# Kernel tuning notes

Measured on AMD Instinct MI355X. Metric: run time of the kernel, lower is better.

Reference implementation:

```python
import jax, jax.numpy as jnp
import numpy as np


def soft_threshold24(w):
    """2:4 soft-threshold along the last dim: in each contiguous group of 4,
    zero the two smallest magnitudes and shrink the two largest by the
    second-smallest magnitude (sign(w) * relu(|w| - t))."""
    M, N = w.shape
    g = w.reshape(M, N // 4, 4)
    a = jnp.abs(g)
    thr = jnp.sort(a, axis=-1)[..., 1:2]  # 2nd-smallest magnitude per group
    s = jnp.sign(g) * jnp.maximum(a - thr, 0.0)
    return s.reshape(M, N)


def mm_fp16(a, b):
    """fake_fp8_mm: cast operands to fp16, accumulate in fp32."""
    return jnp.matmul(a.astype(jnp.float16), b.astype(jnp.float16),
                      preferred_element_type=jnp.float32)


def setup_inputs() -> dict:
    key = jax.random.key(0)
    k0, k1, k2, k3 = jax.random.split(key, 4)
    B, S, D, R = 4, 2048, 2048, 512
    return {
        "x": jax.random.normal(k0, (B, S, D), jnp.float32),
        "weight_in": jax.random.normal(k1, (D, R), jnp.float32) * 0.02,
        "weight_out": jax.random.normal(k2, (D, R), jnp.float32) * 0.02,
        "bias": jax.random.normal(k3, (D,), jnp.float32) * 0.01,
        "sparse_scale_in": jnp.array(1.0, jnp.float32),
        "sparse_scale_out": jnp.array(1.0, jnp.float32),
    }


def reference(x, weight_in, weight_out, bias, sparse_scale_in, sparse_scale_out):
    B, S, D = x.shape
    # stage 1: x @ sparse24(weight_in) * scale_in  -> [B,S,R]
    win_s = soft_threshold24(weight_in) * sparse_scale_in          # [D, R]
    h = mm_fp16(x.reshape(-1, D), win_s)                            # [B*S, R] fp32
    # stage 2: h @ sparse24(weight_out.T) * scale_out + bias -> [B,S,D]
    wout_s = soft_threshold24(weight_out.T) * sparse_scale_out      # [R, D]
    out = mm_fp16(h, wout_s) + bias                                 # [B*S, D]
    return out.reshape(B, S, D)
```

## Files before the change

### kernel.cpp

```cpp
#include <hip/hip_runtime.h>

typedef _Float16 f16;
typedef _Float16 f16x8 __attribute__((ext_vector_type(8)));
typedef float f32x4 __attribute__((ext_vector_type(4)));

#define BK 32

__device__ __forceinline__ void g2l16(const void* g, void* l) {
    __builtin_amdgcn_global_load_lds(
        (const __attribute__((address_space(1))) void*)g,
        (__attribute__((address_space(3))) void*)l, 16, 0, 0);
}

template <int N> __device__ __forceinline__ void wait_vmcnt();
template <> __device__ __forceinline__ void wait_vmcnt<0>() { asm volatile("s_waitcnt vmcnt(0)" ::: "memory"); }
template <> __device__ __forceinline__ void wait_vmcnt<4>() { asm volatile("s_waitcnt vmcnt(4)" ::: "memory"); }

__device__ __forceinline__ float soft1(float a, float thr, float w, float s) {
    return copysignf(fmaxf(a - thr, 0.0f), w) * s;
}

__device__ __forceinline__ float thr4(float a0, float a1, float a2, float a3) {
    float lo01 = fminf(a0, a1), hi01 = fmaxf(a0, a1);
    float lo23 = fminf(a2, a3), hi23 = fmaxf(a2, a3);
    return fminf(fmaxf(lo01, lo23), fminf(hi01, hi23));
}

__global__ __launch_bounds__(256) void prep_kernel(
    const float* __restrict__ Wi, f16* __restrict__ winT, const float* __restrict__ sci,
    const float* __restrict__ Wo, f16* __restrict__ woutT, const float* __restrict__ sco,
    int D, int R, int nSpInB)
{
    int b = blockIdx.x;
    int tid = threadIdx.x;
    if (b < nSpInB) {
        int t = b * 256 + tid;
        int RG = R >> 2;
        if (t >= RG * D) return;
        int rg = t / D, d = t - rg * D;
        float s = *sci;
        float4 w = *reinterpret_cast<const float4*>(Wi + (size_t)d * R + rg * 4);
        float a0 = fabsf(w.x), a1 = fabsf(w.y), a2 = fabsf(w.z), a3 = fabsf(w.w);
        float thr = thr4(a0, a1, a2, a3);
        size_t base = (size_t)(rg * 4) * D + d;
        winT[base]                 = (f16)soft1(a0, thr, w.x, s);
        winT[base + D]             = (f16)soft1(a1, thr, w.y, s);
        winT[base + 2 * (size_t)D] = (f16)soft1(a2, thr, w.z, s);
        winT[base + 3 * (size_t)D] = (f16)soft1(a3, thr, w.w, s);
    } else {
        int t = (b - nSpInB) * 256 + tid;
        if (t >= (D >> 2) * R) return;
        int dg = t / R, r = t - dg * R;
        float s = *sco;
        size_t i0 = (size_t)(dg * 4) * R + r;
        float w0 = Wo[i0], w1 = Wo[i0 + R], w2 = Wo[i0 + 2 * (size_t)R], w3 = Wo[i0 + 3 * (size_t)R];
        float a0 = fabsf(w0), a1 = fabsf(w1), a2 = fabsf(w2), a3 = fabsf(w3);
        float thr = thr4(a0, a1, a2, a3);
        woutT[i0]                 = (f16)soft1(a0, thr, w0, s);
        woutT[i0 + R]             = (f16)soft1(a1, thr, w1, s);
        woutT[i0 + 2 * (size_t)R] = (f16)soft1(a2, thr, w2, s);
        woutT[i0 + 3 * (size_t)R] = (f16)soft1(a3, thr, w3, s);
    }
}

template <int TBM, int TBN, typename AT, typename OT, bool BIAS>
__global__ __launch_bounds__(256) void gemm_bt(
    const AT* __restrict__ A, const f16* __restrict__ Bt, OT* __restrict__ C,
    const float* __restrict__ bias, int M, int N, int K)
{
    constexpr bool AF32 = sizeof(AT) == 4;
    constexpr int MI = TBM / 32;
    constexpr int NF = TBN / 32;
    constexpr int HM = TBM / 2;
    constexpr int HN = TBN / 2;
    constexpr int LA = TBM * BK * (int)sizeof(AT) / 4096;
    constexpr int LB = TBN * BK * 2 / 4096;
    constexpr int L  = LA + LB;
    static_assert(L == 4, "wait_vmcnt<L> instantiations assume L==4");
    __shared__ AT  As[2][TBM * BK];
    __shared__ f16 Bs[2][TBN * BK];

    const int tid  = threadIdx.x;
    const int lane = tid & 63;
    const int w    = tid >> 6;
    const int wm   = w & 1;
    const int wn   = w >> 1;
    const int l16  = lane & 15;
    const int quad = lane >> 4;

    const int nbx = N / TBN;
    const int nb  = gridDim.x;
    int d = blockIdx.x;
    int wgid = ((nb & 7) == 0) ? ((d & 7) * (nb >> 3) + (d >> 3)) : d;
    int by = wgid / nbx;
    int bx = wgid - by * nbx;
    const int bm = by * TBM;
    const int bn = bx * TBN;

    const int srow = lane >> 2;
    const int scol = (lane & 3) * 8;
    const f16* gB = Bt + (size_t)(bn + w * (TBN / 4) + srow) * K + scol;

    const int srowA = AF32 ? (lane >> 3) : srow;
    const int scolA = AF32 ? (((lane & 7) ^ (lane >> 3)) * 4) : scol;
    const AT* gA = A + (size_t)(bm + w * (TBM / 4) + srowA) * K + scolA;

    f32x4 acc[MI][NF] = {};

    auto STAGE = [&](int buf, int t) {
        const int k0 = t * BK;
        AT*  lA = &As[buf][(w * (TBM / 4)) * BK];
        f16* lB = &Bs[buf][(w * (TBN / 4)) * BK];
        if constexpr (AF32) {
#pragma unroll
            for (int i = 0; i < (TBM / 4) / 8; ++i)
                g2l16(gA + k0 + i * 8 * (size_t)K, lA + i * 8 * BK);
        } else {
#pragma unroll
            for (int i = 0; i < (TBM / 4) / 16; ++i)
                g2l16(gA + k0 + i * 16 * (size_t)K, lA + i * 16 * BK);
        }
#pragma unroll
        for (int i = 0; i < (TBN / 4) / 16; ++i)
            g2l16(gB + k0 + i * 16 * (size_t)K, lB + i * 16 * BK);
    };

    auto LOADFRAG = [&](int buf, f16x8* af, f16x8* bf) {
        if constexpr (AF32) {
#pragma unroll
            for (int m = 0; m < MI; ++m) {
                int lr = wm * HM + m * 16 + l16;
                const char* row = reinterpret_cast<const char*>(&As[buf][lr * BK]);
                int swz = (lr & 7) << 4;
                f32x4 lo = *reinterpret_cast<const f32x4*>(row + (((quad * 32)      ) ^ swz));
                f32x4 hi = *reinterpret_cast<const f32x4*>(row + (((quad * 32) + 16 ) ^ swz));
                f16x8 a;
#pragma unroll
                for (int j = 0; j < 4; ++j) { a[j] = (f16)lo[j]; a[j + 4] = (f16)hi[j]; }
                af[m] = a;
            }
        } else {
#pragma unroll
            for (int m = 0; m < MI; ++m)
                af[m] = *reinterpret_cast<const f16x8*>(
                    &As[buf][(wm * HM + m * 16 + l16) * BK + quad * 8]);
        }
#pragma unroll
        for (int n = 0; n < NF; ++n)
            bf[n] = *reinterpret_cast<const f16x8*>(
                &Bs[buf][(wn * HN + n * 16 + l16) * BK + quad * 8]);
    };

    auto MFMA_ALL = [&](f16x8* af, f16x8* bf) {
#pragma unroll
        for (int m = 0; m < MI; ++m)
#pragma unroll
            for (int n = 0; n < NF; ++n)
                acc[m][n] = __builtin_amdgcn_mfma_f32_16x16x32_f16(af[m], bf[n], acc[m][n], 0, 0, 0);
    };

    const int nk = K / BK;
    STAGE(0, 0);
    STAGE(1, 1);
    for (int t = 0; t < nk - 2; ++t) {
        wait_vmcnt<4>();
        __builtin_amdgcn_s_barrier();
        __builtin_amdgcn_sched_barrier(0);
        f16x8 af[MI], bf[NF];
        LOADFRAG(t & 1, af, bf);
        asm volatile("s_waitcnt lgkmcnt(0)" ::: "memory");
        __builtin_amdgcn_sched_barrier(0);
        __builtin_amdgcn_s_barrier();
        STAGE(t & 1, t + 2);
        MFMA_ALL(af, bf);
    }
    {
        wait_vmcnt<4>();
        __builtin_amdgcn_s_barrier();
        __builtin_amdgcn_sched_barrier(0);
        f16x8 af[MI], bf[NF];
        LOADFRAG(nk & 1, af, bf);
        MFMA_ALL(af, bf);
    }
    {
        wait_vmcnt<0>();
        __builtin_amdgcn_s_barrier();
        __builtin_amdgcn_sched_barrier(0);
        f16x8 af[MI], bf[NF];
        LOADFRAG((nk - 1) & 1, af, bf);
        MFMA_ALL(af, bf);
    }

#pragma unroll
    for (int m = 0; m < MI; ++m) {
        int row_base = bm + wm * HM + m * 16 + quad * 4;
#pragma unroll
        for (int n = 0; n < NF; ++n) {
            int col = bn + wn * HN + n * 16 + l16;
            float b = BIAS ? bias[col] : 0.0f;
#pragma unroll
            for (int r = 0; r < 4; ++r) {
                float v = acc[m][n][r];
                size_t idx = (size_t)(row_base + r) * N + col;
                if constexpr (BIAS) C[idx] = (OT)(v + b);
                else                C[idx] = (OT)v;
            }
        }
    }
}

extern "C" void kernel_launch(void* const* d_in, const int* in_sizes, int n_in,
                              void* d_out, int out_size, void* d_ws, size_t ws_size,
                              hipStream_t stream)
{
    const float* x      = (const float*)d_in[0];
    const float* w_in   = (const float*)d_in[1];
    const float* w_out  = (const float*)d_in[2];
    const float* bias   = (const float*)d_in[3];
    const float* sc_in  = (const float*)d_in[4];
    const float* sc_out = (const float*)d_in[5];

    const int D = in_sizes[3];
    const int R = in_sizes[1] / D;
    const int M = in_sizes[0] / D;

    f16* winT  = (f16*)d_ws;
    f16* woutT = winT + (size_t)R * D;
    f16* h     = woutT + (size_t)D * R;
    float* out = (float*)d_out;

    const int nSpInB  = ((R / 4) * D + 255) / 256;
    const int nSpOutB = ((D / 4) * R + 255) / 256;
    prep_kernel<<<nSpInB + nSpOutB, 256, 0, stream>>>(
        w_in, winT, sc_in, w_out, woutT, sc_out, D, R, nSpInB);

    gemm_bt<64, 128, float, f16, false><<<(R / 128) * (M / 64), 256, 0, stream>>>(
        x, winT, h, nullptr, M, R, D);
    gemm_bt<128, 128, f16, float, true><<<(D / 128) * (M / 128), 256, 0, stream>>>(
        h, woutT, out, bias, M, D, R);
}
```

Before: 197.6 us.

## Stage fp32 A via registers, converting to fp16 before LDS write

For the fp32-input GEMM (stage 1), A tiles are no longer copied straight from global memory into LDS as fp32. They are now loaded into registers, converted to fp16 once, and written to LDS as fp16. This halves the LDS footprint and LDS read traffic for A, and removes the repeated per-fragment fp32-to-fp16 conversion. In exchange it adds register staging, a manually unrolled two-buffer loop with extra barriers and lgkmcnt waits, and loses the asynchronous direct-to-LDS path for A.

```diff
diff --git a/kernel.cpp b/kernel.cpp
--- a/kernel.cpp
+++ b/kernel.cpp
@@ -73,11 +73,7 @@
     constexpr int NF = TBN / 32;
     constexpr int HM = TBM / 2;
     constexpr int HN = TBN / 2;
-    constexpr int LA = TBM * BK * (int)sizeof(AT) / 4096;
-    constexpr int LB = TBN * BK * 2 / 4096;
-    constexpr int L  = LA + LB;
-    static_assert(L == 4, "wait_vmcnt<L> instantiations assume L==4");
-    __shared__ AT  As[2][TBM * BK];
+    __shared__ f16 As[2][TBM * BK];
     __shared__ f16 Bs[2][TBN * BK];
 
     const int tid  = threadIdx.x;
@@ -100,51 +96,23 @@
     const int srow = lane >> 2;
     const int scol = (lane & 3) * 8;
     const f16* gB = Bt + (size_t)(bn + w * (TBN / 4) + srow) * K + scol;
-
-    const int srowA = AF32 ? (lane >> 3) : srow;
-    const int scolA = AF32 ? (((lane & 7) ^ (lane >> 3)) * 4) : scol;
-    const AT* gA = A + (size_t)(bm + w * (TBM / 4) + srowA) * K + scolA;
+    const AT*  gA = A  + (size_t)(bm + w * (TBM / 4) + srow) * K + scol;
+    const int  aoff = (w * (TBM / 4) + srow) * BK + scol;
 
     f32x4 acc[MI][NF] = {};
 
-    auto STAGE = [&](int buf, int t) {
-        const int k0 = t * BK;
-        AT*  lA = &As[buf][(w * (TBM / 4)) * BK];
+    auto STAGE_B = [&](int buf, int t) {
         f16* lB = &Bs[buf][(w * (TBN / 4)) * BK];
-        if constexpr (AF32) {
-#pragma unroll
-            for (int i = 0; i < (TBM / 4) / 8; ++i)
-                g2l16(gA + k0 + i * 8 * (size_t)K, lA + i * 8 * BK);
-        } else {
-#pragma unroll
-            for (int i = 0; i < (TBM / 4) / 16; ++i)
-                g2l16(gA + k0 + i * 16 * (size_t)K, lA + i * 16 * BK);
-        }
 #pragma unroll
         for (int i = 0; i < (TBN / 4) / 16; ++i)
-            g2l16(gB + k0 + i * 16 * (size_t)K, lB + i * 16 * BK);
+            g2l16(gB + (size_t)t * BK + i * 16 * (size_t)K, lB + i * 16 * BK);
     };
 
     auto LOADFRAG = [&](int buf, f16x8* af, f16x8* bf) {
-        if constexpr (AF32) {
-#pragma unroll
-            for (int m = 0; m < MI; ++m) {
-                int lr = wm * HM + m * 16 + l16;
-                const char* row = reinterpret_cast<const char*>(&As[buf][lr * BK]);
-                int swz = (lr & 7) << 4;
-                f32x4 lo = *reinterpret_cast<const f32x4*>(row + (((quad * 32)      ) ^ swz));
-                f32x4 hi = *reinterpret_cast<const f32x4*>(row + (((quad * 32) + 16 ) ^ swz));
-                f16x8 a;
-#pragma unroll
-                for (int j = 0; j < 4; ++j) { a[j] = (f16)lo[j]; a[j + 4] = (f16)hi[j]; }
-                af[m] = a;
-            }
-        } else {
-#pragma unroll
-            for (int m = 0; m < MI; ++m)
-                af[m] = *reinterpret_cast<const f16x8*>(
-                    &As[buf][(wm * HM + m * 16 + l16) * BK + quad * 8]);
-        }
+#pragma unroll
+        for (int m = 0; m < MI; ++m)
+            af[m] = *reinterpret_cast<const f16x8*>(
+                &As[buf][(wm * HM + m * 16 + l16) * BK + quad * 8]);
 #pragma unroll
         for (int n = 0; n < NF; ++n)
             bf[n] = *reinterpret_cast<const f16x8*>(
@@ -160,35 +128,121 @@
     };
 
     const int nk = K / BK;
-    STAGE(0, 0);
-    STAGE(1, 1);
-    for (int t = 0; t < nk - 2; ++t) {
-        wait_vmcnt<4>();
-        __builtin_amdgcn_s_barrier();
+
+    if constexpr (AF32) {
+        auto ALOAD = [&](int t, f32x4& r0, f32x4& r1) {
+            const float* p = (const float*)gA + (size_t)t * BK;
+            r0 = *reinterpret_cast<const f32x4*>(p);
+            r1 = *reinterpret_cast<const f32x4*>(p + 4);
+        };
+        auto AWRITE = [&](int buf, const f32x4& r0, const f32x4& r1) {
+            f16x8 v;
+#pragma unroll
+            for (int j = 0; j < 4; ++j) { v[j] = (f16)r0[j]; v[j + 4] = (f16)r1[j]; }
+            *reinterpret_cast<f16x8*>(&As[buf][aoff]) = v;
+        };
+        f32x4 a0E, a1E, a0O, a1O;
+        ALOAD(0, a0E, a1E); STAGE_B(0, 0);
         __builtin_amdgcn_sched_barrier(0);
-        f16x8 af[MI], bf[NF];
-        LOADFRAG(t & 1, af, bf);
-        asm volatile("s_waitcnt lgkmcnt(0)" ::: "memory");
+        ALOAD(1, a0O, a1O); STAGE_B(1, 1);
         __builtin_amdgcn_sched_barrier(0);
-        __builtin_amdgcn_s_barrier();
-        STAGE(t & 1, t + 2);
-        MFMA_ALL(af, bf);
-    }
-    {
-        wait_vmcnt<4>();
-        __builtin_amdgcn_s_barrier();
-        __builtin_amdgcn_sched_barrier(0);
-        f16x8 af[MI], bf[NF];
-        LOADFRAG(nk & 1, af, bf);
-        MFMA_ALL(af, bf);
-    }
-    {
-        wait_vmcnt<0>();
-        __builtin_amdgcn_s_barrier();
-        __builtin_amdgcn_sched_barrier(0);
-        f16x8 af[MI], bf[NF];
-        LOADFRAG((nk - 1) & 1, af, bf);
-        MFMA_ALL(af, bf);
+        for (int t = 0; t < nk - 2; t += 2) {
+            wait_vmcnt<4>();
+            __builtin_amdgcn_sched_barrier(0);
+            AWRITE(0, a0E, a1E);
+            asm volatile("s_waitcnt lgkmcnt(0)" ::: "memory");
+            __builtin_amdgcn_sched_barrier(0);
+            __builtin_amdgcn_s_barrier();
+            f16x8 af[MI], bf[NF];
+            LOADFRAG(0, af, bf);
+            asm volatile("s_waitcnt lgkmcnt(0)" ::: "memory");
+            __builtin_amdgcn_sched_barrier(0);
+            __builtin_amdgcn_s_barrier();
+            ALOAD(t + 2, a0E, a1E); STAGE_B(0, t + 2);
+            __builtin_amdgcn_sched_barrier(0);
+            MFMA_ALL(af, bf);
+            wait_vmcnt<4>();
+            __builtin_amdgcn_sched_barrier(0);
+            AWRITE(1, a0O, a1O);
+            asm volatile("s_waitcnt lgkmcnt(0)" ::: "memory");
+            __builtin_amdgcn_sched_barrier(0);
+            __builtin_amdgcn_s_barrier();
+            LOADFRAG(1, af, bf);
+            asm volatile("s_waitcnt lgkmcnt(0)" ::: "memory");
+            __builtin_amdgcn_sched_barrier(0);
+            __builtin_amdgcn_s_barrier();
+            ALOAD(t + 3, a0O, a1O); STAGE_B(1, t + 3);
+            __builtin_amdgcn_sched_barrier(0);
+            MFMA_ALL(af, bf);
+        }
+        {
+            wait_vmcnt<4>();
+            __builtin_amdgcn_sched_barrier(0);
+            AWRITE(0, a0E, a1E);
+            asm volatile("s_waitcnt lgkmcnt(0)" ::: "memory");
+            __builtin_amdgcn_sched_barrier(0);
+            __builtin_amdgcn_s_barrier();
+            f16x8 af[MI], bf[NF];
+            LOADFRAG(0, af, bf);
+            asm volatile("s_waitcnt lgkmcnt(0)" ::: "memory");
+            __builtin_amdgcn_sched_barrier(0);
+            MFMA_ALL(af, bf);
+        }
+        {
+            wait_vmcnt<0>();
+            __builtin_amdgcn_sched_barrier(0);
+            AWRITE(1, a0O, a1O);
+            asm volatile("s_waitcnt lgkmcnt(0)" ::: "memory");
+            __builtin_amdgcn_sched_barrier(0);
+            __builtin_amdgcn_s_barrier();
+            f16x8 af[MI], bf[NF];
+            LOADFRAG(1, af, bf);
+            asm volatile("s_waitcnt lgkmcnt(0)" ::: "memory");
+            __builtin_amdgcn_sched_barrier(0);
+            MFMA_ALL(af, bf);
+        }
+    } else {
+        auto STAGE = [&](int buf, int t) {
+            f16* lA = &As[buf][(w * (TBM / 4)) * BK];
+#pragma unroll
+            for (int i = 0; i < (TBM / 4) / 16; ++i)
+                g2l16((const f16*)gA + (size_t)t * BK + i * 16 * (size_t)K, lA + i * 16 * BK);
+            STAGE_B(buf, t);
+        };
+        STAGE(0, 0);
+        STAGE(1, 1);
+        for (int t = 0; t < nk - 2; ++t) {
+            wait_vmcnt<4>();
+            __builtin_amdgcn_s_barrier();
+            __builtin_amdgcn_sched_barrier(0);
+            f16x8 af[MI], bf[NF];
+            LOADFRAG(t & 1, af, bf);
+            asm volatile("s_waitcnt lgkmcnt(0)" ::: "memory");
+            __builtin_amdgcn_sched_barrier(0);
+            __builtin_amdgcn_s_barrier();
+            STAGE(t & 1, t + 2);
+            MFMA_ALL(af, bf);
+        }
+        {
+            wait_vmcnt<4>();
+            __builtin_amdgcn_s_barrier();
+            __builtin_amdgcn_sched_barrier(0);
+            f16x8 af[MI], bf[NF];
+            LOADFRAG(nk & 1, af, bf);
+            asm volatile("s_waitcnt lgkmcnt(0)" ::: "memory");
+            __builtin_amdgcn_sched_barrier(0);
+            MFMA_ALL(af, bf);
+        }
+        {
+            wait_vmcnt<0>();
+            __builtin_amdgcn_s_barrier();
+            __builtin_amdgcn_sched_barrier(0);
+            f16x8 af[MI], bf[NF];
+            LOADFRAG((nk - 1) & 1, af, bf);
+            asm volatile("s_waitcnt lgkmcnt(0)" ::: "memory");
+            __builtin_amdgcn_sched_barrier(0);
+            MFMA_ALL(af, bf);
+        }
     }
 
 #pragma unroll
```

New measurement: 193.2 us. -2.2%, faster.
